# Optimization experiments

Hardware: AMD Instinct MI355X
Metric: run time of the kernel (lower is better)

## Reference

```python
import jax, jax.numpy as jnp
import numpy as np

BATCH = 1024
FEAT_DIM = 128
NUM_CLASSES = 100000
MARGIN = 0.1
SCALAR = 1.0
EPS = 1e-12


def setup_inputs() -> dict:
    key = jax.random.key(0)
    k1, k2, k3 = jax.random.split(key, 3)
    inputs = jax.random.normal(k1, (BATCH, FEAT_DIM), dtype=jnp.float32)
    targets = jax.random.randint(k2, (BATCH,), 0, NUM_CLASSES, dtype=jnp.int32)
    # LUT buffer: unit-norm rows (as maintained by the momentum/renorm update)
    lut = jax.random.normal(k3, (NUM_CLASSES, FEAT_DIM), dtype=jnp.float32)
    lut = lut / (jnp.linalg.norm(lut, axis=-1, keepdims=True) + EPS)
    return {"inputs": inputs, "targets": targets, "lut": lut}


def reference(inputs, targets, lut):
    # L2-normalize features (normalize_feature=True path)
    x = inputs / (jnp.linalg.norm(inputs, axis=-1, keepdims=True) + EPS)
    # logits against the memory bank: [B, C]
    logits = x @ lut.T
    # additive margin on the target class only, then scale
    rows = jnp.arange(logits.shape[0])
    logits = logits.at[rows, targets].add(-MARGIN)
    logits = logits * SCALAR
    # cross entropy, mean reduction (label_smooth=False path)
    logp = jax.nn.log_softmax(logits, axis=-1)
    loss = -jnp.mean(logp[rows, targets])
    return loss, logits
```

## Files before the change

### kernel.cpp

```cpp
#include <hip/hip_runtime.h>
#include <cstdint>
#include <cstddef>

#define BATCH 1024
#define FEAT 128
#define NCLS 100000
#define MARGIN 0.1f
#define SCALARV 1.0f
#define EPSV 1e-12f

#define BN 160
#define NBLOCKS 625

typedef __bf16 bf16x8 __attribute__((ext_vector_type(8)));
typedef float floatx4 __attribute__((ext_vector_type(4)));

#define WS_X 0
#define WS_SUMEXP 262144
#define WS_TLOGIT 266240

static __device__ __forceinline__ unsigned short f2bf(float f) {
    uint32_t u = __float_as_uint(f);
    u += 0x7FFFu + ((u >> 16) & 1u);
    return (unsigned short)(u >> 16);
}

__global__ __launch_bounds__(256) void k_normalize(const float* __restrict__ in,
                                                   unsigned short* __restrict__ xb,
                                                   float* __restrict__ sumexp) {
    if (blockIdx.x == 0) {
        for (int i = threadIdx.x; i < BATCH; i += 256) sumexp[i] = 0.0f;
    }
    const int wid = threadIdx.x >> 6;
    const int lane = threadIdx.x & 63;
    const int row = blockIdx.x * 4 + wid;
    const float2 v = reinterpret_cast<const float2*>(in + (size_t)row * FEAT)[lane];
    float ss = v.x * v.x + v.y * v.y;
#pragma unroll
    for (int m = 1; m <= 32; m <<= 1) ss += __shfl_xor(ss, m, 64);
    const float scale = 1.0f / (sqrtf(ss) + EPSV);
    const unsigned int lo = f2bf(v.x * scale);
    const unsigned int hi = f2bf(v.y * scale);
    reinterpret_cast<unsigned int*>(xb + (size_t)row * FEAT)[lane] = lo | (hi << 16);
}

__global__ __launch_bounds__(256, 2) void k_gemm(const unsigned short* __restrict__ xb,
                                                 const float* __restrict__ lut,
                                                 const int* __restrict__ targets,
                                                 float* __restrict__ out_logits,
                                                 float* __restrict__ sumexp,
                                                 float* __restrict__ tlogit) {
    const int n0 = blockIdx.x * BN;
    const int tid = threadIdx.x;
    const int wid = tid >> 6;
    const int lane = tid & 63;
    const int q = lane >> 4;
    const int c = lane & 15;
    const int wm = wid >> 1;
    const int wn = wid & 1;

    bf16x8 bfrag[5][4];
#pragma unroll
    for (int ni = 0; ni < 5; ++ni) {
        const int nrow = n0 + wn * 80 + ni * 16 + c;
        const float* bp = lut + (size_t)nrow * FEAT;
#pragma unroll
        for (int ks = 0; ks < 4; ++ks) {
            const int k = ks * 32 + q * 8;
            const floatx4 f0 = __builtin_nontemporal_load(
                reinterpret_cast<const floatx4*>(bp + k));
            const floatx4 f1 = __builtin_nontemporal_load(
                reinterpret_cast<const floatx4*>(bp + k) + 1);
            union { unsigned short s[8]; bf16x8 v; } t;
            t.s[0] = f2bf(f0[0]); t.s[1] = f2bf(f0[1]);
            t.s[2] = f2bf(f0[2]); t.s[3] = f2bf(f0[3]);
            t.s[4] = f2bf(f1[0]); t.s[5] = f2bf(f1[1]);
            t.s[6] = f2bf(f1[2]); t.s[7] = f2bf(f1[3]);
            bfrag[ni][ks] = t.v;
        }
    }

    for (int miter = 0; miter < 8; ++miter) {
        const int m0 = miter * 128;
        floatx4 acc[4][5];
#pragma unroll
        for (int mi = 0; mi < 4; ++mi)
#pragma unroll
            for (int ni = 0; ni < 5; ++ni) {
                floatx4 z = {0.0f, 0.0f, 0.0f, 0.0f};
                acc[mi][ni] = z;
            }

#pragma unroll
        for (int ks = 0; ks < 4; ++ks) {
            bf16x8 af[4];
#pragma unroll
            for (int mi = 0; mi < 4; ++mi) {
                const int mrow = m0 + wm * 64 + mi * 16 + c;
                af[mi] = *reinterpret_cast<const bf16x8*>(
                    xb + (size_t)mrow * FEAT + ks * 32 + q * 8);
            }
#pragma unroll
            for (int mi = 0; mi < 4; ++mi)
#pragma unroll
                for (int ni = 0; ni < 5; ++ni)
                    acc[mi][ni] = __builtin_amdgcn_mfma_f32_16x16x32_bf16(
                        bfrag[ni][ks], af[mi], acc[mi][ni], 0, 0, 0);
        }

#pragma unroll
        for (int mi = 0; mi < 4; ++mi) {
            const int row = m0 + wm * 64 + mi * 16 + c;
            const int tgt = targets[row];
            float* rowp = out_logits + (size_t)row * NCLS;
            float part = 0.0f;
#pragma unroll
            for (int ni = 0; ni < 5; ++ni) {
                const int nb = n0 + wn * 80 + ni * 16 + q * 4;
                floatx4 vv = acc[mi][ni];
#pragma unroll
                for (int r = 0; r < 4; ++r) {
                    float v = vv[r];
                    const bool hit = (nb + r == tgt);
                    if (hit) v -= MARGIN;
                    v *= SCALARV;
                    if (hit) tlogit[row] = v;
                    vv[r] = v;
                    part += __expf(v);
                }
                *reinterpret_cast<floatx4*>(rowp + nb) = vv;
            }
            part += __shfl_xor(part, 16, 64);
            part += __shfl_xor(part, 32, 64);
            if (q == 0) atomicAdd(&sumexp[row], part);
        }
    }
}

__global__ __launch_bounds__(1024) void k_loss(const float* __restrict__ sumexp,
                                               const float* __restrict__ tlogit,
                                               float* __restrict__ out) {
    __shared__ float wsum[16];
    const int tid = threadIdx.x;
    float v = logf(sumexp[tid]) - tlogit[tid];
#pragma unroll
    for (int m = 1; m <= 32; m <<= 1) v += __shfl_xor(v, m, 64);
    if ((tid & 63) == 0) wsum[tid >> 6] = v;
    __syncthreads();
    if (tid < 64) {
        float t = (tid < 16) ? wsum[tid] : 0.0f;
#pragma unroll
        for (int m = 1; m <= 8; m <<= 1) t += __shfl_xor(t, m, 64);
        if (tid == 0) out[0] = t * (1.0f / BATCH);
    }
}

extern "C" void kernel_launch(void* const* d_in, const int* in_sizes, int n_in,
                              void* d_out, int out_size, void* d_ws, size_t ws_size,
                              hipStream_t stream) {
    const float* inputs = (const float*)d_in[0];
    const int* targets = (const int*)d_in[1];
    const float* lut = (const float*)d_in[2];

    float* out = (float*)d_out;
    char* ws = (char*)d_ws;
    unsigned short* xb = (unsigned short*)(ws + WS_X);
    float* sumexp = (float*)(ws + WS_SUMEXP);
    float* tlogit = (float*)(ws + WS_TLOGIT);

    k_normalize<<<BATCH / 4, 256, 0, stream>>>(inputs, xb, sumexp);
    k_gemm<<<NBLOCKS, 256, 0, stream>>>(xb, lut, targets, out + 1, sumexp, tlogit);
    k_loss<<<1, 1024, 0, stream>>>(sumexp, tlogit, out);
}
```

Before: 580.2 us.

## Split GEMM over M halves and replace sumexp atomics with partial buffer reduction

Doubles the GEMM grid by splitting the batch rows into two halves per N tile, so more blocks fill the CUs. Per-row sum-of-exp atomics are replaced by writes into a per-row partial buffer, which a new row-reduce kernel sums before a final mean kernel. This removes atomic contention. In exchange, each LUT tile is loaded and converted twice, two extra launches are added, and the partial path only runs when the workspace is large enough (about 5 MB), otherwise it falls back to the old path.

```diff
diff --git a/kernel.cpp b/kernel.cpp
--- a/kernel.cpp
+++ b/kernel.cpp
@@ -10,14 +10,22 @@
 #define EPSV 1e-12f
 
 #define BN 160
-#define NBLOCKS 625
+#define NTILES 625
+#define MSPLIT 2
+#define NBLOCKS (NTILES * MSPLIT)
+#define MROWS (BATCH / MSPLIT)
+#define PCOLS (NTILES * 2)
+#define PSTRIDE 1280
 
 typedef __bf16 bf16x8 __attribute__((ext_vector_type(8)));
 typedef float floatx4 __attribute__((ext_vector_type(4)));
 
 #define WS_X 0
-#define WS_SUMEXP 262144
-#define WS_TLOGIT 266240
+#define WS_TLOGIT 262144
+#define WS_ROWVAL 266240
+#define WS_SUMEXP 270336
+#define WS_PARTIAL 274432
+#define WS_NEEDED (WS_PARTIAL + (size_t)BATCH * PSTRIDE * 4)
 
 static __device__ __forceinline__ unsigned short f2bf(float f) {
     uint32_t u = __float_as_uint(f);
@@ -27,9 +35,19 @@
 
 __global__ __launch_bounds__(256) void k_normalize(const float* __restrict__ in,
                                                    unsigned short* __restrict__ xb,
-                                                   float* __restrict__ sumexp) {
-    if (blockIdx.x == 0) {
-        for (int i = threadIdx.x; i < BATCH; i += 256) sumexp[i] = 0.0f;
+                                                   float* __restrict__ aux,
+                                                   int partial_mode) {
+    const int t = blockIdx.x * 256 + threadIdx.x;
+    if (partial_mode) {
+        if (t < BATCH * (PSTRIDE - PCOLS)) {
+            const int row = t / (PSTRIDE - PCOLS);
+            const int j = t - row * (PSTRIDE - PCOLS);
+            aux[(size_t)row * PSTRIDE + PCOLS + j] = 0.0f;
+        }
+    } else {
+        if (blockIdx.x == 0) {
+            for (int i = threadIdx.x; i < BATCH; i += 256) aux[i] = 0.0f;
+        }
     }
     const int wid = threadIdx.x >> 6;
     const int lane = threadIdx.x & 63;
@@ -44,13 +62,18 @@
     reinterpret_cast<unsigned int*>(xb + (size_t)row * FEAT)[lane] = lo | (hi << 16);
 }
 
+template <int PARTIAL>
 __global__ __launch_bounds__(256, 2) void k_gemm(const unsigned short* __restrict__ xb,
                                                  const float* __restrict__ lut,
                                                  const int* __restrict__ targets,
                                                  float* __restrict__ out_logits,
-                                                 float* __restrict__ sumexp,
+                                                 float* __restrict__ aux,
                                                  float* __restrict__ tlogit) {
-    const int n0 = blockIdx.x * BN;
+    const int bid = blockIdx.x;
+    const int ntile = PARTIAL ? (bid >> 1) : bid;
+    const int mbase = PARTIAL ? ((bid & 1) * MROWS) : 0;
+    const int nmiter = PARTIAL ? (MROWS / 128) : (BATCH / 128);
+    const int n0 = ntile * BN;
     const int tid = threadIdx.x;
     const int wid = tid >> 6;
     const int lane = tid & 63;
@@ -80,8 +103,8 @@
         }
     }
 
-    for (int miter = 0; miter < 8; ++miter) {
-        const int m0 = miter * 128;
+    for (int miter = 0; miter < nmiter; ++miter) {
+        const int m0 = mbase + miter * 128;
         floatx4 acc[4][5];
 #pragma unroll
         for (int mi = 0; mi < 4; ++mi)
@@ -132,8 +155,49 @@
             }
             part += __shfl_xor(part, 16, 64);
             part += __shfl_xor(part, 32, 64);
-            if (q == 0) atomicAdd(&sumexp[row], part);
-        }
+            if (q == 0) {
+                if (PARTIAL) {
+                    aux[(size_t)row * PSTRIDE + ntile * 2 + wn] = part;
+                } else {
+                    atomicAdd(&aux[row], part);
+                }
+            }
+        }
+    }
+}
+
+__global__ __launch_bounds__(256) void k_rowreduce(const float* __restrict__ partial,
+                                                   const float* __restrict__ tlogit,
+                                                   float* __restrict__ rowval) {
+    const int wid = threadIdx.x >> 6;
+    const int lane = threadIdx.x & 63;
+    const int row = blockIdx.x * 4 + wid;
+    const floatx4* p = reinterpret_cast<const floatx4*>(partial + (size_t)row * PSTRIDE);
+    float s = 0.0f;
+#pragma unroll
+    for (int i = 0; i < PSTRIDE / 256; ++i) {
+        const floatx4 v = p[lane + i * 64];
+        s += v[0] + v[1] + v[2] + v[3];
+    }
+#pragma unroll
+    for (int m = 1; m <= 32; m <<= 1) s += __shfl_xor(s, m, 64);
+    if (lane == 0) rowval[row] = logf(s) - tlogit[row];
+}
+
+__global__ __launch_bounds__(1024) void k_mean(const float* __restrict__ rowval,
+                                               float* __restrict__ out) {
+    __shared__ float wsum[16];
+    const int tid = threadIdx.x;
+    float v = rowval[tid];
+#pragma unroll
+    for (int m = 1; m <= 32; m <<= 1) v += __shfl_xor(v, m, 64);
+    if ((tid & 63) == 0) wsum[tid >> 6] = v;
+    __syncthreads();
+    if (tid < 64) {
+        float t = (tid < 16) ? wsum[tid] : 0.0f;
+#pragma unroll
+        for (int m = 1; m <= 8; m <<= 1) t += __shfl_xor(t, m, 64);
+        if (tid == 0) out[0] = t * (1.0f / BATCH);
     }
 }
 
@@ -165,10 +229,20 @@
     float* out = (float*)d_out;
     char* ws = (char*)d_ws;
     unsigned short* xb = (unsigned short*)(ws + WS_X);
+    float* tlogit = (float*)(ws + WS_TLOGIT);
+    float* rowval = (float*)(ws + WS_ROWVAL);
     float* sumexp = (float*)(ws + WS_SUMEXP);
-    float* tlogit = (float*)(ws + WS_TLOGIT);
-
-    k_normalize<<<BATCH / 4, 256, 0, stream>>>(inputs, xb, sumexp);
-    k_gemm<<<NBLOCKS, 256, 0, stream>>>(xb, lut, targets, out + 1, sumexp, tlogit);
-    k_loss<<<1, 1024, 0, stream>>>(sumexp, tlogit, out);
-}
+    float* partial = (float*)(ws + WS_PARTIAL);
+
+    const bool use_partial = (ws_size >= WS_NEEDED);
+    if (use_partial) {
+        k_normalize<<<BATCH / 4, 256, 0, stream>>>(inputs, xb, partial, 1);
+        k_gemm<1><<<NBLOCKS, 256, 0, stream>>>(xb, lut, targets, out + 1, partial, tlogit);
+        k_rowreduce<<<BATCH / 4, 256, 0, stream>>>(partial, tlogit, rowval);
+        k_mean<<<1, 1024, 0, stream>>>(rowval, out);
+    } else {
+        k_normalize<<<BATCH / 4, 256, 0, stream>>>(inputs, xb, sumexp, 0);
+        k_gemm<0><<<NTILES, 256, 0, stream>>>(xb, lut, targets, out + 1, sumexp, tlogit);
+        k_loss<<<1, 1024, 0, stream>>>(sumexp, tlogit, out);
+    }
+}
```

After: 580.5 us. No clear change (+0.1%).
